# Kernel optimization log

Measured on AMD Instinct MI355X. Metric: run time of the kernel, lower is better.

Reference implementation:

```python
import jax, jax.numpy as jnp
import numpy as np

B, U, CV, IN, H = 256, 64, 61, 3, 1024
NG, NAG = 20, 10
G = 4 * H  # LSTM gate width (i,f,g,o)


def _lstm_cell(x, h, c, Wih, Whh, bih, bhh):
    # PyTorch LSTM gate order: i, f, g, o
    g = x @ Wih.T + h @ Whh.T + bih + bhh
    i, f, gg, o = jnp.split(g, 4, axis=-1)
    c2 = jax.nn.sigmoid(f) * c + jax.nn.sigmoid(i) * jnp.tanh(gg)
    h2 = jax.nn.sigmoid(o) * jnp.tanh(c2)
    return h2, c2


def _bilstm(x, h, c, pf, pb):
    # Bidirectional LSTM over a length-1 sequence: one cell step per direction.
    hf, cf = _lstm_cell(x, h[0], c[0], *pf)
    hb, cb = _lstm_cell(x, h[1], c[1], *pb)
    return jnp.concatenate([hf, hb], axis=-1), jnp.stack([hf, hb]), jnp.stack([cf, cb])


def _forward(inp, char_vec, old_k, old_w, h1, c1, h2, c2, params, text_len):
    (Wih1f, Whh1f, bih1f, bhh1f, Wih1b, Whh1b, bih1b, bhh1b,
     Wih2f, Whh2f, bih2f, bhh2f, Wih2b, Whh2b, bih2b, bhh2b,
     W_win, b_win, W_mdn, b_mdn) = params
    # embed = cat([inp, old_w]) over the feature dim; seq len is 1 so squeeze it.
    x1 = jnp.concatenate([inp[:, 0], old_w[:, 0]], axis=-1)          # [B, IN+CV]
    out1, h1n, c1n = _bilstm(x1, h1, c1,
                             (Wih1f, Whh1f, bih1f, bhh1f),
                             (Wih1b, Whh1b, bih1b, bhh1b))           # [B, 2H]
    # Gaussian-mixture attention window (Graves 2013)
    abk = jnp.exp(out1 @ W_win.T + b_win)                            # [B, 3*NAG]
    a_t, b_t, k_t = jnp.split(abk, 3, axis=1)
    k_t = old_k + k_t
    u = jnp.arange(1, U + 1, dtype=jnp.float32)                      # [U]
    phi_bku = jnp.exp(-b_t[:, :, None] * (k_t[:, :, None] - u) ** 2) # [B,NAG,U]
    phi = jnp.einsum('bk,bku->bu', a_t, phi_bku) * (float(U) / text_len)
    win = jnp.einsum('bu,buc->bc', phi, char_vec)                    # [B, CV]
    # Second LSTM with skip connections
    x2 = jnp.concatenate([out1, inp[:, 0], win], axis=-1)            # [B, 2H+IN+CV]
    out2, h2n, c2n = _bilstm(x2, h2, c2,
                             (Wih2f, Whh2f, bih2f, bhh2f),
                             (Wih2b, Whh2b, bih2b, bhh2b))           # [B, 2H]
    # Mixture-density output head
    y = jnp.concatenate([out1, out2], axis=-1) @ W_mdn.T + b_mdn     # [B, 6*NG+1]
    e = jax.nn.sigmoid(y[:, :1])
    pi, mu1, mu2, s1, s2, rho = jnp.split(y[:, 1:], 6, axis=1)
    pi = jax.nn.softmax(pi, axis=1)  # bias = 0 default
    return (e, pi, mu1, mu2, jnp.exp(s1), jnp.exp(s2), jnp.tanh(rho),
            phi, win, k_t, h1n, c1n, h2n, c2n)


def setup_inputs() -> dict:
    key = jax.random.key(0)
    ks = jax.random.split(key, 32)
    def w(k, shape):
        return jax.random.normal(k, shape, dtype=jnp.float32) * 0.02
    d = {
        'inp': jax.random.normal(ks[0], (B, 1, IN), dtype=jnp.float32),
        'char_vec': jax.random.uniform(ks[1], (B, U, CV), dtype=jnp.float32),
        'old_k': jax.random.uniform(ks[2], (B, NAG), dtype=jnp.float32),
        'old_w': jax.random.uniform(ks[3], (B, 1, CV), dtype=jnp.float32),
        'h1': jnp.zeros((2, B, H), jnp.float32),
        'c1': jnp.zeros((2, B, H), jnp.float32),
        'h2': jnp.zeros((2, B, H), jnp.float32),
        'c2': jnp.zeros((2, B, H), jnp.float32),
        'text_len': 64,
    }
    in1 = IN + CV          # rnn1 input width = 64
    in2 = 2 * H + IN + CV  # rnn2 input width = 2112
    i = 4
    for pre, ind in [('1f', in1), ('1b', in1), ('2f', in2), ('2b', in2)]:
        d['Wih' + pre] = w(ks[i], (G, ind)); i += 1
        d['Whh' + pre] = w(ks[i], (G, H)); i += 1
        d['bih' + pre] = w(ks[i], (G,)); i += 1
        d['bhh' + pre] = w(ks[i], (G,)); i += 1
    d['W_win'] = w(ks[i], (3 * NAG, 2 * H)); i += 1
    d['b_win'] = w(ks[i], (3 * NAG,)) - 2.0; i += 1  # keep exp(abk) moderate
    d['W_mdn'] = w(ks[i], (6 * NG + 1, 4 * H)); i += 1
    d['b_mdn'] = w(ks[i], (6 * NG + 1,))
    return d


def reference(inp, char_vec, old_k, old_w, h1, c1, h2, c2, text_len,
              Wih1f, Whh1f, bih1f, bhh1f, Wih1b, Whh1b, bih1b, bhh1b,
              Wih2f, Whh2f, bih2f, bhh2f, Wih2b, Whh2b, bih2b, bhh2b,
              W_win, b_win, W_mdn, b_mdn):
    params = (Wih1f, Whh1f, bih1f, bhh1f, Wih1b, Whh1b, bih1b, bhh1b,
              Wih2f, Whh2f, bih2f, bhh2f, Wih2b, Whh2b, bih2b, bhh2b,
              W_win, b_win, W_mdn, b_mdn)
    return _forward(inp, char_vec, old_k, old_w, h1, c1, h2, c2, params, text_len)
```

## Files before the change

### kernel.cpp

```cpp
#include <hip/hip_runtime.h>

#define Bsz 256
#define Usz 64
#define CVsz 61
#define INsz 3
#define Hsz 1024
#define Gsz 4096
#define NGsz 20
#define NAGsz 10
#define IN2sz 2112

typedef __attribute__((ext_vector_type(8))) short bf16x8;
typedef __attribute__((ext_vector_type(4))) float f32x4;
typedef __attribute__((ext_vector_type(4))) unsigned int u32x4;

__device__ __forceinline__ unsigned int pk2(float x, float y) {
  unsigned int a = __float_as_uint(x), b = __float_as_uint(y);
  return ((a + 0x8000u) >> 16) | ((b + 0x8000u) & 0xffff0000u);
}

__device__ __forceinline__ float sigf(float x) { return 1.f / (1.f + __expf(-x)); }

struct GemmP {
  const float* X1; int ldx1; int nc1; int ldw1;
  const float* Wf1; const float* Wb1;
  const float* Hst; const float* Wf2; const float* Wb2;
  const float* bihf; const float* bhhf; const float* bihb; const float* bhhb;
  float* gout;
  int ksplit; int totc; int ndir; int nW; int ldo;
};

__global__ __launch_bounds__(256) void gemm_k(GemmP p) {
  __shared__ __align__(16) unsigned short As[128 * 32];
  __shared__ __align__(16) unsigned short Bs[128 * 32];
  int t = threadIdx.x;
  int n0 = blockIdx.x * 128, m0 = blockIdx.y * 128;
  int z = blockIdx.z;
  int d = (p.ndir == 2) ? (z & 1) : 0;
  int s = (p.ndir == 2) ? (z >> 1) : z;
  const float* Wih = d ? p.Wb1 : p.Wf1;
  const float* Whh = d ? p.Wb2 : p.Wf2;
  const float* Hx = p.Hst + (size_t)d * Bsz * Hsz;
  int c0 = (p.totc * s) / p.ksplit, c1 = (p.totc * (s + 1)) / p.ksplit;
  int wv = t >> 6, ln = t & 63;
  int wr = wv >> 1, wc = wv & 1;
  int fr = ln & 15, kg = ln >> 4;
  int sr = t >> 1, skp = (t & 1) * 16;

  f32x4 acc[4][4];
#pragma unroll
  for (int i = 0; i < 4; i++)
#pragma unroll
    for (int j = 0; j < 4; j++) acc[i][j] = (f32x4){0.f, 0.f, 0.f, 0.f};

  for (int c = c0; c < c1; ++c) {
    const float* Xp; int ldx, kx; const float* Wp; int ldw;
    if (c < p.nc1) { Xp = p.X1; ldx = p.ldx1; kx = c * 32; Wp = Wih; ldw = p.ldw1; }
    else           { Xp = Hx;   ldx = Hsz;    kx = (c - p.nc1) * 32; Wp = Whh; ldw = Hsz; }

    const float* ax = Xp + (size_t)(m0 + sr) * ldx + kx + skp;
    float4 a0 = *(const float4*)(ax);
    float4 a1 = *(const float4*)(ax + 4);
    float4 a2 = *(const float4*)(ax + 8);
    float4 a3 = *(const float4*)(ax + 12);
    int rw = n0 + sr; if (rw >= p.nW) rw = p.nW - 1;
    const float* bx = Wp + (size_t)rw * ldw + kx + skp;
    float4 b0 = *(const float4*)(bx);
    float4 b1 = *(const float4*)(bx + 4);
    float4 b2 = *(const float4*)(bx + 8);
    float4 b3 = *(const float4*)(bx + 12);

    __syncthreads();
    *(u32x4*)(&As[sr * 32 + skp])     = (u32x4){pk2(a0.x, a0.y), pk2(a0.z, a0.w), pk2(a1.x, a1.y), pk2(a1.z, a1.w)};
    *(u32x4*)(&As[sr * 32 + skp + 8]) = (u32x4){pk2(a2.x, a2.y), pk2(a2.z, a2.w), pk2(a3.x, a3.y), pk2(a3.z, a3.w)};
    *(u32x4*)(&Bs[sr * 32 + skp])     = (u32x4){pk2(b0.x, b0.y), pk2(b0.z, b0.w), pk2(b1.x, b1.y), pk2(b1.z, b1.w)};
    *(u32x4*)(&Bs[sr * 32 + skp + 8]) = (u32x4){pk2(b2.x, b2.y), pk2(b2.z, b2.w), pk2(b3.x, b3.y), pk2(b3.z, b3.w)};
    __syncthreads();

    const unsigned short* Ab = &As[(wr * 64 + fr) * 32 + kg * 8];
    const unsigned short* Bb = &Bs[(wc * 64 + fr) * 32 + kg * 8];
    bf16x8 av[4], bv[4];
#pragma unroll
    for (int i = 0; i < 4; i++) av[i] = *(const bf16x8*)(Ab + i * 16 * 32);
#pragma unroll
    for (int j = 0; j < 4; j++) bv[j] = *(const bf16x8*)(Bb + j * 16 * 32);
#pragma unroll
    for (int i = 0; i < 4; i++)
#pragma unroll
      for (int j = 0; j < 4; j++)
        acc[i][j] = __builtin_amdgcn_mfma_f32_16x16x32_bf16(av[i], bv[j], acc[i][j], 0, 0, 0);
  }

  const float* bi = d ? p.bihb : p.bihf;
  const float* bh = d ? p.bhhb : p.bhhf;
  float* outp = p.gout + (size_t)(s * p.ndir + d) * Bsz * p.ldo;
#pragma unroll
  for (int i = 0; i < 4; i++) {
#pragma unroll
    for (int j = 0; j < 4; j++) {
      int col = n0 + wc * 64 + j * 16 + fr;
      float bias = 0.f;
      if (p.bihf && s == 0) bias = bi[col] + bh[col];
#pragma unroll
      for (int r = 0; r < 4; r++) {
        int row = m0 + wr * 64 + i * 16 + kg * 4 + r;
        outp[(size_t)row * p.ldo + col] = acc[i][j][r] + bias;
      }
    }
  }
}

__global__ __launch_bounds__(256) void prep_x1(const float* inp, const float* oldw, float* x1) {
  int idx = blockIdx.x * 256 + threadIdx.x;
  int m = idx >> 6, k = idx & 63;
  x1[idx] = (k < INsz) ? inp[m * INsz + k] : oldw[m * CVsz + (k - INsz)];
}

__global__ __launch_bounds__(256) void cell_k(const float* gates, int ksplit,
    const float* cin, float* hout, float* cout,
    float* dst1, int ld1, int off1, float* dst2, int ld2, int off2) {
  int idx = blockIdx.x * 256 + threadIdx.x;
  int j = idx & (Hsz - 1);
  int m = (idx >> 10) & 255;
  int d = idx >> 18;
  size_t base = ((size_t)d * Bsz + m) * Gsz + j;
  float gi = 0.f, gf = 0.f, gg = 0.f, go = 0.f;
  for (int s = 0; s < ksplit; ++s) {
    const float* gp = gates + (size_t)s * 2 * Bsz * Gsz + base;
    gi += gp[0]; gf += gp[1024]; gg += gp[2048]; go += gp[3072];
  }
  float c = cin[((size_t)d * Bsz + m) * Hsz + j];
  float cn = sigf(gf) * c + sigf(gi) * tanhf(gg);
  float hn = sigf(go) * tanhf(cn);
  hout[((size_t)d * Bsz + m) * Hsz + j] = hn;
  cout[((size_t)d * Bsz + m) * Hsz + j] = cn;
  dst1[(size_t)m * ld1 + off1 + d * Hsz + j] = hn;
  if (dst2) dst2[(size_t)m * ld2 + off2 + d * Hsz + j] = hn;
}

__global__ __launch_bounds__(128) void win_fin(const float* winp, int ks,
    const float* bwin, const float* oldk, const float* inp, const float* cvec,
    const int* tl, float* x2w, float* ophi, float* owin, float* okt) {
  int m = blockIdx.x, t = threadIdx.x, wv = t >> 6, ln = t & 63;
  __shared__ float abk[30];
  __shared__ float phis[Usz];
  __shared__ float wpart[2][CVsz];
  if (t < 30) {
    float s = bwin[t];
    for (int q = 0; q < ks; ++q) s += winp[((size_t)q * Bsz + m) * 128 + t];
    abk[t] = __expf(s);
  }
  __syncthreads();
  if (t < NAGsz) {
    float kt = oldk[m * NAGsz + t] + abk[20 + t];
    abk[20 + t] = kt;
    okt[m * NAGsz + t] = kt;
  }
  __syncthreads();
  if (t < Usz) {
    float scale = 64.f / (float)tl[0];
    float ph = 0.f;
#pragma unroll
    for (int q = 0; q < NAGsz; ++q) {
      float dk = abk[20 + q] - (float)(t + 1);
      ph += abk[q] * __expf(-abk[10 + q] * dk * dk);
    }
    ph *= scale;
    phis[t] = ph;
    ophi[m * Usz + t] = ph;
  }
  __syncthreads();
  if (ln < CVsz) {
    float w = 0.f;
    const float* cv = cvec + (size_t)m * Usz * CVsz + (size_t)wv * 32 * CVsz + ln;
#pragma unroll
    for (int u = 0; u < 32; ++u) w += phis[wv * 32 + u] * cv[u * CVsz];
    wpart[wv][ln] = w;
  }
  __syncthreads();
  if (t < CVsz) {
    float w = wpart[0][t] + wpart[1][t];
    owin[m * CVsz + t] = w;
    x2w[(size_t)m * IN2sz + 2048 + INsz + t] = w;
  }
  if (t < INsz) x2w[(size_t)m * IN2sz + 2048 + t] = inp[m * INsz + t];
}

__global__ __launch_bounds__(128) void mdn_fin(const float* part, int ks, const float* bm, float* out) {
  int m = blockIdx.x, t = threadIdx.x;
  __shared__ float y[121];
  if (t < 121) {
    float s = bm[t];
    for (int q = 0; q < ks; ++q) s += part[((size_t)q * Bsz + m) * 128 + t];
    y[t] = s;
  }
  __syncthreads();
  if (t == 0) out[m] = sigf(y[0]);
  if (t < NGsz) {
    float mx = -1e30f;
    for (int q = 0; q < NGsz; q++) mx = fmaxf(mx, y[1 + q]);
    float se = 0.f;
    for (int q = 0; q < NGsz; q++) se += __expf(y[1 + q] - mx);
    out[256   + m * NGsz + t] = __expf(y[1 + t] - mx) / se;
    out[5376  + m * NGsz + t] = y[21 + t];
    out[10496 + m * NGsz + t] = y[41 + t];
    out[15616 + m * NGsz + t] = __expf(y[61 + t]);
    out[20736 + m * NGsz + t] = __expf(y[81 + t]);
    out[25856 + m * NGsz + t] = tanhf(y[101 + t]);
  }
}

extern "C" void kernel_launch(void* const* d_in, const int* in_sizes, int n_in,
                              void* d_out, int out_size, void* d_ws, size_t ws_size,
                              hipStream_t stream) {
  (void)in_sizes; (void)n_in; (void)out_size;
  const float* inp  = (const float*)d_in[0];
  const float* cvec = (const float*)d_in[1];
  const float* oldk = (const float*)d_in[2];
  const float* oldw = (const float*)d_in[3];
  const float* h1   = (const float*)d_in[4];
  const float* c1   = (const float*)d_in[5];
  const float* h2   = (const float*)d_in[6];
  const float* c2   = (const float*)d_in[7];
  const int*   tl   = (const int*)d_in[8];
  float* out = (float*)d_out;
  float* ws  = (float*)d_ws;

  float* ws_x1   = ws;
  float* ws_x2   = ws + 16384;
  float* ws_cat  = ws_x2 + 540672;
  float* ws_mdn  = ws_cat + 1048576;
  float* ws_winp = ws_mdn + 262144;
  float* ws_g    = ws_winp + 262144;

  size_t fixed = (size_t)16384 + 540672 + 1048576 + 262144 + 262144;
  int ksplit = 4;
  while (ksplit > 1 && (fixed + (size_t)ksplit * 2 * 1048576) * 4 > ws_size) ksplit >>= 1;

  prep_x1<<<64, 256, 0, stream>>>(inp, oldw, ws_x1);

  GemmP g1{};
  g1.X1 = ws_x1; g1.ldx1 = 64; g1.nc1 = 2; g1.ldw1 = 64;
  g1.Wf1 = (const float*)d_in[9];  g1.Wb1 = (const float*)d_in[13];
  g1.Hst = h1; g1.Wf2 = (const float*)d_in[10]; g1.Wb2 = (const float*)d_in[14];
  g1.bihf = (const float*)d_in[11]; g1.bhhf = (const float*)d_in[12];
  g1.bihb = (const float*)d_in[15]; g1.bhhb = (const float*)d_in[16];
  g1.gout = ws_g; g1.ksplit = ksplit; g1.totc = 34; g1.ndir = 2; g1.nW = 4096; g1.ldo = 4096;
  gemm_k<<<dim3(32, 2, 2 * ksplit), 256, 0, stream>>>(g1);

  cell_k<<<2048, 256, 0, stream>>>(ws_g, ksplit, c1, out + 65536, out + 589824,
                                   ws_x2, IN2sz, 0, ws_cat, 4096, 0);

  GemmP gw{};
  gw.X1 = ws_x2; gw.ldx1 = IN2sz; gw.nc1 = 64; gw.ldw1 = 2048;
  gw.Wf1 = (const float*)d_in[25]; gw.Wb1 = (const float*)d_in[25];
  gw.Hst = ws_x2; gw.Wf2 = (const float*)d_in[25]; gw.Wb2 = (const float*)d_in[25];
  gw.bihf = nullptr; gw.bhhf = nullptr; gw.bihb = nullptr; gw.bhhb = nullptr;
  gw.gout = ws_winp; gw.ksplit = 8; gw.totc = 64; gw.ndir = 1; gw.nW = 30; gw.ldo = 128;
  gemm_k<<<dim3(1, 2, 8), 256, 0, stream>>>(gw);

  win_fin<<<256, 128, 0, stream>>>(ws_winp, 8, (const float*)d_in[26],
                                   oldk, inp, cvec, tl, ws_x2,
                                   out + 30976, out + 47360, out + 62976);

  GemmP g2{};
  g2.X1 = ws_x2; g2.ldx1 = IN2sz; g2.nc1 = 66; g2.ldw1 = IN2sz;
  g2.Wf1 = (const float*)d_in[17]; g2.Wb1 = (const float*)d_in[21];
  g2.Hst = h2; g2.Wf2 = (const float*)d_in[18]; g2.Wb2 = (const float*)d_in[22];
  g2.bihf = (const float*)d_in[19]; g2.bhhf = (const float*)d_in[20];
  g2.bihb = (const float*)d_in[23]; g2.bhhb = (const float*)d_in[24];
  g2.gout = ws_g; g2.ksplit = ksplit; g2.totc = 98; g2.ndir = 2; g2.nW = 4096; g2.ldo = 4096;
  gemm_k<<<dim3(32, 2, 2 * ksplit), 256, 0, stream>>>(g2);

  cell_k<<<2048, 256, 0, stream>>>(ws_g, ksplit, c2, out + 1114112, out + 1638400,
                                   ws_cat, 4096, 2048, nullptr, 0, 0);

  GemmP gm{};
  gm.X1 = ws_cat; gm.ldx1 = 4096; gm.nc1 = 128; gm.ldw1 = 4096;
  gm.Wf1 = (const float*)d_in[27]; gm.Wb1 = (const float*)d_in[27];
  gm.Hst = ws_cat; gm.Wf2 = ws_cat; gm.Wb2 = ws_cat;
  gm.bihf = nullptr; gm.bhhf = nullptr; gm.bihb = nullptr; gm.bhhb = nullptr;
  gm.gout = ws_mdn; gm.ksplit = 8; gm.totc = 128; gm.ndir = 1; gm.nW = 121; gm.ldo = 128;
  gemm_k<<<dim3(1, 2, 8), 256, 0, stream>>>(gm);

  mdn_fin<<<256, 128, 0, stream>>>(ws_mdn, 8, (const float*)d_in[28], out);
}
```

Baseline: 314.6 us.

## Double-buffer GEMM shared tiles with padding and raise split-K factors

The GEMM main loop now uses two padded LDS buffers. The global loads for the next K chunk are issued before the MFMA work on the current chunk, and only one barrier is needed per iteration. Row padding to 40 elements is meant to cut LDS bank conflicts on the fragment reads. Split-K doubles for the LSTM gate GEMMs and the small window and MDN GEMMs to put more blocks in flight. This costs larger workspace partials and more reduction traffic in the cell and finalize kernels.

```diff
diff --git a/kernel.cpp b/kernel.cpp
--- a/kernel.cpp
+++ b/kernel.cpp
@@ -9,6 +9,7 @@
 #define NGsz 20
 #define NAGsz 10
 #define IN2sz 2112
+#define LDP 40
 
 typedef __attribute__((ext_vector_type(8))) short bf16x8;
 typedef __attribute__((ext_vector_type(4))) float f32x4;
@@ -30,9 +31,9 @@
   int ksplit; int totc; int ndir; int nW; int ldo;
 };
 
-__global__ __launch_bounds__(256) void gemm_k(GemmP p) {
-  __shared__ __align__(16) unsigned short As[128 * 32];
-  __shared__ __align__(16) unsigned short Bs[128 * 32];
+__global__ __launch_bounds__(256, 4) void gemm_k(GemmP p) {
+  __shared__ __align__(16) unsigned short As[2][128 * LDP];
+  __shared__ __align__(16) unsigned short Bs[2][128 * LDP];
   int t = threadIdx.x;
   int n0 = blockIdx.x * 128, m0 = blockIdx.y * 128;
   int z = blockIdx.z;
@@ -53,43 +54,57 @@
 #pragma unroll
     for (int j = 0; j < 4; j++) acc[i][j] = (f32x4){0.f, 0.f, 0.f, 0.f};
 
-  for (int c = c0; c < c1; ++c) {
+  float4 a0, a1, a2, a3, b0, b1, b2, b3;
+
+  auto LOAD = [&](int c) {
     const float* Xp; int ldx, kx; const float* Wp; int ldw;
     if (c < p.nc1) { Xp = p.X1; ldx = p.ldx1; kx = c * 32; Wp = Wih; ldw = p.ldw1; }
     else           { Xp = Hx;   ldx = Hsz;    kx = (c - p.nc1) * 32; Wp = Whh; ldw = Hsz; }
-
     const float* ax = Xp + (size_t)(m0 + sr) * ldx + kx + skp;
-    float4 a0 = *(const float4*)(ax);
-    float4 a1 = *(const float4*)(ax + 4);
-    float4 a2 = *(const float4*)(ax + 8);
-    float4 a3 = *(const float4*)(ax + 12);
+    a0 = *(const float4*)(ax);
+    a1 = *(const float4*)(ax + 4);
+    a2 = *(const float4*)(ax + 8);
+    a3 = *(const float4*)(ax + 12);
     int rw = n0 + sr; if (rw >= p.nW) rw = p.nW - 1;
     const float* bx = Wp + (size_t)rw * ldw + kx + skp;
-    float4 b0 = *(const float4*)(bx);
-    float4 b1 = *(const float4*)(bx + 4);
-    float4 b2 = *(const float4*)(bx + 8);
-    float4 b3 = *(const float4*)(bx + 12);
-
-    __syncthreads();
-    *(u32x4*)(&As[sr * 32 + skp])     = (u32x4){pk2(a0.x, a0.y), pk2(a0.z, a0.w), pk2(a1.x, a1.y), pk2(a1.z, a1.w)};
-    *(u32x4*)(&As[sr * 32 + skp + 8]) = (u32x4){pk2(a2.x, a2.y), pk2(a2.z, a2.w), pk2(a3.x, a3.y), pk2(a3.z, a3.w)};
-    *(u32x4*)(&Bs[sr * 32 + skp])     = (u32x4){pk2(b0.x, b0.y), pk2(b0.z, b0.w), pk2(b1.x, b1.y), pk2(b1.z, b1.w)};
-    *(u32x4*)(&Bs[sr * 32 + skp + 8]) = (u32x4){pk2(b2.x, b2.y), pk2(b2.z, b2.w), pk2(b3.x, b3.y), pk2(b3.z, b3.w)};
-    __syncthreads();
-
-    const unsigned short* Ab = &As[(wr * 64 + fr) * 32 + kg * 8];
-    const unsigned short* Bb = &Bs[(wc * 64 + fr) * 32 + kg * 8];
+    b0 = *(const float4*)(bx);
+    b1 = *(const float4*)(bx + 4);
+    b2 = *(const float4*)(bx + 8);
+    b3 = *(const float4*)(bx + 12);
+  };
+  auto STORE = [&](int buf) {
+    *(u32x4*)(&As[buf][sr * LDP + skp])     = (u32x4){pk2(a0.x, a0.y), pk2(a0.z, a0.w), pk2(a1.x, a1.y), pk2(a1.z, a1.w)};
+    *(u32x4*)(&As[buf][sr * LDP + skp + 8]) = (u32x4){pk2(a2.x, a2.y), pk2(a2.z, a2.w), pk2(a3.x, a3.y), pk2(a3.z, a3.w)};
+    *(u32x4*)(&Bs[buf][sr * LDP + skp])     = (u32x4){pk2(b0.x, b0.y), pk2(b0.z, b0.w), pk2(b1.x, b1.y), pk2(b1.z, b1.w)};
+    *(u32x4*)(&Bs[buf][sr * LDP + skp + 8]) = (u32x4){pk2(b2.x, b2.y), pk2(b2.z, b2.w), pk2(b3.x, b3.y), pk2(b3.z, b3.w)};
+  };
+  auto MFMA = [&](int buf) {
+    const unsigned short* Ab = &As[buf][(wr * 64 + fr) * LDP + kg * 8];
+    const unsigned short* Bb = &Bs[buf][(wc * 64 + fr) * LDP + kg * 8];
     bf16x8 av[4], bv[4];
 #pragma unroll
-    for (int i = 0; i < 4; i++) av[i] = *(const bf16x8*)(Ab + i * 16 * 32);
-#pragma unroll
-    for (int j = 0; j < 4; j++) bv[j] = *(const bf16x8*)(Bb + j * 16 * 32);
+    for (int i = 0; i < 4; i++) av[i] = *(const bf16x8*)(Ab + i * 16 * LDP);
+#pragma unroll
+    for (int j = 0; j < 4; j++) bv[j] = *(const bf16x8*)(Bb + j * 16 * LDP);
 #pragma unroll
     for (int i = 0; i < 4; i++)
 #pragma unroll
       for (int j = 0; j < 4; j++)
         acc[i][j] = __builtin_amdgcn_mfma_f32_16x16x32_bf16(av[i], bv[j], acc[i][j], 0, 0, 0);
-  }
+  };
+
+  LOAD(c0);
+  STORE(0);
+  __syncthreads();
+  int cur = 0;
+  for (int c = c0 + 1; c < c1; ++c) {
+    LOAD(c);
+    MFMA(cur);
+    STORE(cur ^ 1);
+    __syncthreads();
+    cur ^= 1;
+  }
+  MFMA(cur);
 
   const float* bi = d ? p.bihb : p.bihf;
   const float* bh = d ? p.bhhb : p.bhhf;
@@ -230,11 +245,11 @@
   float* ws_x2   = ws + 16384;
   float* ws_cat  = ws_x2 + 540672;
   float* ws_mdn  = ws_cat + 1048576;
-  float* ws_winp = ws_mdn + 262144;
-  float* ws_g    = ws_winp + 262144;
-
-  size_t fixed = (size_t)16384 + 540672 + 1048576 + 262144 + 262144;
-  int ksplit = 4;
+  float* ws_winp = ws_mdn + 524288;
+  float* ws_g    = ws_winp + 524288;
+
+  size_t fixed = (size_t)16384 + 540672 + 1048576 + 524288 + 524288;
+  int ksplit = 8;
   while (ksplit > 1 && (fixed + (size_t)ksplit * 2 * 1048576) * 4 > ws_size) ksplit >>= 1;
 
   prep_x1<<<64, 256, 0, stream>>>(inp, oldw, ws_x1);
@@ -256,10 +271,10 @@
   gw.Wf1 = (const float*)d_in[25]; gw.Wb1 = (const float*)d_in[25];
   gw.Hst = ws_x2; gw.Wf2 = (const float*)d_in[25]; gw.Wb2 = (const float*)d_in[25];
   gw.bihf = nullptr; gw.bhhf = nullptr; gw.bihb = nullptr; gw.bhhb = nullptr;
-  gw.gout = ws_winp; gw.ksplit = 8; gw.totc = 64; gw.ndir = 1; gw.nW = 30; gw.ldo = 128;
-  gemm_k<<<dim3(1, 2, 8), 256, 0, stream>>>(gw);
-
-  win_fin<<<256, 128, 0, stream>>>(ws_winp, 8, (const float*)d_in[26],
+  gw.gout = ws_winp; gw.ksplit = 16; gw.totc = 64; gw.ndir = 1; gw.nW = 30; gw.ldo = 128;
+  gemm_k<<<dim3(1, 2, 16), 256, 0, stream>>>(gw);
+
+  win_fin<<<256, 128, 0, stream>>>(ws_winp, 16, (const float*)d_in[26],
                                    oldk, inp, cvec, tl, ws_x2,
                                    out + 30976, out + 47360, out + 62976);
 
@@ -280,8 +295,8 @@
   gm.Wf1 = (const float*)d_in[27]; gm.Wb1 = (const float*)d_in[27];
   gm.Hst = ws_cat; gm.Wf2 = ws_cat; gm.Wb2 = ws_cat;
   gm.bihf = nullptr; gm.bhhf = nullptr; gm.bihb = nullptr; gm.bhhb = nullptr;
-  gm.gout = ws_mdn; gm.ksplit = 8; gm.totc = 128; gm.ndir = 1; gm.nW = 121; gm.ldo = 128;
-  gemm_k<<<dim3(1, 2, 8), 256, 0, stream>>>(gm);
-
-  mdn_fin<<<256, 128, 0, stream>>>(ws_mdn, 8, (const float*)d_in[28], out);
-}
+  gm.gout = ws_mdn; gm.ksplit = 16; gm.totc = 128; gm.ndir = 1; gm.nW = 121; gm.ldo = 128;
+  gemm_k<<<dim3(1, 2, 16), 256, 0, stream>>>(gm);
+
+  mdn_fin<<<256, 128, 0, stream>>>(ws_mdn, 16, (const float*)d_in[28], out);
+}
```

Measured after the change: 336.9 us. 1.07x slower.

## Double-buffer GEMM LDS tiles with K=64 chunks, padding and register prefetch

Applied to the files above, without the earlier changes.

The GEMM kernel now processes 64-wide K chunks instead of 32, uses double-buffered padded LDS tiles (stride 72 to reduce bank conflicts), and prefetches the next chunk's global loads into registers while MFMAs run on the current buffer, leaving one barrier per iteration. Chunk counts in the host launches are halved to match, and the first LSTM GEMM uses a smaller k-split. The aim is to hide global-load latency and cut synchronisation overhead. In exchange it needs more registers (16 float4 staging) and more LDS, which may limit occupancy despite the launch bound hint.

```diff
diff --git a/kernel.cpp b/kernel.cpp
--- a/kernel.cpp
+++ b/kernel.cpp
@@ -9,6 +9,7 @@
 #define NGsz 20
 #define NAGsz 10
 #define IN2sz 2112
+#define LDP 72
 
 typedef __attribute__((ext_vector_type(8))) short bf16x8;
 typedef __attribute__((ext_vector_type(4))) float f32x4;
@@ -30,9 +31,9 @@
   int ksplit; int totc; int ndir; int nW; int ldo;
 };
 
-__global__ __launch_bounds__(256) void gemm_k(GemmP p) {
-  __shared__ __align__(16) unsigned short As[128 * 32];
-  __shared__ __align__(16) unsigned short Bs[128 * 32];
+__global__ __launch_bounds__(256, 2) void gemm_k(GemmP p) {
+  __shared__ __align__(16) unsigned short As[2][128 * LDP];
+  __shared__ __align__(16) unsigned short Bs[2][128 * LDP];
   int t = threadIdx.x;
   int n0 = blockIdx.x * 128, m0 = blockIdx.y * 128;
   int z = blockIdx.z;
@@ -45,7 +46,7 @@
   int wv = t >> 6, ln = t & 63;
   int wr = wv >> 1, wc = wv & 1;
   int fr = ln & 15, kg = ln >> 4;
-  int sr = t >> 1, skp = (t & 1) * 16;
+  int srow = t >> 1, shalf = t & 1;
 
   f32x4 acc[4][4];
 #pragma unroll
@@ -53,43 +54,67 @@
 #pragma unroll
     for (int j = 0; j < 4; j++) acc[i][j] = (f32x4){0.f, 0.f, 0.f, 0.f};
 
-  for (int c = c0; c < c1; ++c) {
+  float4 ar[8], br[8];
+
+  auto LOADR = [&](int c) {
     const float* Xp; int ldx, kx; const float* Wp; int ldw;
-    if (c < p.nc1) { Xp = p.X1; ldx = p.ldx1; kx = c * 32; Wp = Wih; ldw = p.ldw1; }
-    else           { Xp = Hx;   ldx = Hsz;    kx = (c - p.nc1) * 32; Wp = Whh; ldw = Hsz; }
-
-    const float* ax = Xp + (size_t)(m0 + sr) * ldx + kx + skp;
-    float4 a0 = *(const float4*)(ax);
-    float4 a1 = *(const float4*)(ax + 4);
-    float4 a2 = *(const float4*)(ax + 8);
-    float4 a3 = *(const float4*)(ax + 12);
-    int rw = n0 + sr; if (rw >= p.nW) rw = p.nW - 1;
-    const float* bx = Wp + (size_t)rw * ldw + kx + skp;
-    float4 b0 = *(const float4*)(bx);
-    float4 b1 = *(const float4*)(bx + 4);
-    float4 b2 = *(const float4*)(bx + 8);
-    float4 b3 = *(const float4*)(bx + 12);
-
+    if (c < p.nc1) { Xp = p.X1; ldx = p.ldx1; kx = c * 64; Wp = Wih; ldw = p.ldw1; }
+    else           { Xp = Hx;   ldx = Hsz;    kx = (c - p.nc1) * 64; Wp = Whh; ldw = Hsz; }
+    const float* ax = Xp + (size_t)(m0 + srow) * ldx + kx + shalf * 32;
+#pragma unroll
+    for (int q = 0; q < 8; q++) ar[q] = *(const float4*)(ax + 4 * q);
+    int rw = n0 + srow; if (rw >= p.nW) rw = p.nW - 1;
+    const float* bx = Wp + (size_t)rw * ldw + kx + shalf * 32;
+#pragma unroll
+    for (int q = 0; q < 8; q++) br[q] = *(const float4*)(bx + 4 * q);
+  };
+  auto DSW = [&](int buf) {
+    unsigned short* pa = &As[buf][srow * LDP + shalf * 32];
+    unsigned short* pb = &Bs[buf][srow * LDP + shalf * 32];
+#pragma unroll
+    for (int q = 0; q < 4; q++) {
+      *(u32x4*)(pa + q * 8) = (u32x4){pk2(ar[2*q].x, ar[2*q].y), pk2(ar[2*q].z, ar[2*q].w),
+                                      pk2(ar[2*q+1].x, ar[2*q+1].y), pk2(ar[2*q+1].z, ar[2*q+1].w)};
+    }
+#pragma unroll
+    for (int q = 0; q < 4; q++) {
+      *(u32x4*)(pb + q * 8) = (u32x4){pk2(br[2*q].x, br[2*q].y), pk2(br[2*q].z, br[2*q].w),
+                                      pk2(br[2*q+1].x, br[2*q+1].y), pk2(br[2*q+1].z, br[2*q+1].w)};
+    }
+  };
+  auto MFMA = [&](int buf) {
+    const unsigned short* Ab = &As[buf][(wr * 64 + fr) * LDP + kg * 8];
+    const unsigned short* Bb = &Bs[buf][(wc * 64 + fr) * LDP + kg * 8];
+    bf16x8 av[2][4], bv[2][4];
+#pragma unroll
+    for (int kk = 0; kk < 2; kk++) {
+#pragma unroll
+      for (int i = 0; i < 4; i++) av[kk][i] = *(const bf16x8*)(Ab + i * 16 * LDP + kk * 32);
+#pragma unroll
+      for (int j = 0; j < 4; j++) bv[kk][j] = *(const bf16x8*)(Bb + j * 16 * LDP + kk * 32);
+    }
+#pragma unroll
+    for (int kk = 0; kk < 2; kk++)
+#pragma unroll
+      for (int i = 0; i < 4; i++)
+#pragma unroll
+        for (int j = 0; j < 4; j++)
+          acc[i][j] = __builtin_amdgcn_mfma_f32_16x16x32_bf16(av[kk][i], bv[kk][j], acc[i][j], 0, 0, 0);
+  };
+
+  LOADR(c0);
+  DSW(0);
+  __syncthreads();
+  int cur = 0;
+  for (int c = c0 + 1; c < c1; ++c) {
+    LOADR(c);
+    __builtin_amdgcn_sched_barrier(0);
+    MFMA(cur);
+    DSW(cur ^ 1);
     __syncthreads();
-    *(u32x4*)(&As[sr * 32 + skp])     = (u32x4){pk2(a0.x, a0.y), pk2(a0.z, a0.w), pk2(a1.x, a1.y), pk2(a1.z, a1.w)};
-    *(u32x4*)(&As[sr * 32 + skp + 8]) = (u32x4){pk2(a2.x, a2.y), pk2(a2.z, a2.w), pk2(a3.x, a3.y), pk2(a3.z, a3.w)};
-    *(u32x4*)(&Bs[sr * 32 + skp])     = (u32x4){pk2(b0.x, b0.y), pk2(b0.z, b0.w), pk2(b1.x, b1.y), pk2(b1.z, b1.w)};
-    *(u32x4*)(&Bs[sr * 32 + skp + 8]) = (u32x4){pk2(b2.x, b2.y), pk2(b2.z, b2.w), pk2(b3.x, b3.y), pk2(b3.z, b3.w)};
-    __syncthreads();
-
-    const unsigned short* Ab = &As[(wr * 64 + fr) * 32 + kg * 8];
-    const unsigned short* Bb = &Bs[(wc * 64 + fr) * 32 + kg * 8];
-    bf16x8 av[4], bv[4];
-#pragma unroll
-    for (int i = 0; i < 4; i++) av[i] = *(const bf16x8*)(Ab + i * 16 * 32);
-#pragma unroll
-    for (int j = 0; j < 4; j++) bv[j] = *(const bf16x8*)(Bb + j * 16 * 32);
-#pragma unroll
-    for (int i = 0; i < 4; i++)
-#pragma unroll
-      for (int j = 0; j < 4; j++)
-        acc[i][j] = __builtin_amdgcn_mfma_f32_16x16x32_bf16(av[i], bv[j], acc[i][j], 0, 0, 0);
-  }
+    cur ^= 1;
+  }
+  MFMA(cur);
 
   const float* bi = d ? p.bihb : p.bihf;
   const float* bh = d ? p.bhhb : p.bhhf;
@@ -234,29 +259,30 @@
   float* ws_g    = ws_winp + 262144;
 
   size_t fixed = (size_t)16384 + 540672 + 1048576 + 262144 + 262144;
-  int ksplit = 4;
-  while (ksplit > 1 && (fixed + (size_t)ksplit * 2 * 1048576) * 4 > ws_size) ksplit >>= 1;
+  int ks2 = 4;
+  while (ks2 > 1 && (fixed + (size_t)ks2 * 2 * 1048576) * 4 > ws_size) ks2 >>= 1;
+  int ks1 = ks2 < 2 ? 1 : 2;
 
   prep_x1<<<64, 256, 0, stream>>>(inp, oldw, ws_x1);
 
   GemmP g1{};
-  g1.X1 = ws_x1; g1.ldx1 = 64; g1.nc1 = 2; g1.ldw1 = 64;
+  g1.X1 = ws_x1; g1.ldx1 = 64; g1.nc1 = 1; g1.ldw1 = 64;
   g1.Wf1 = (const float*)d_in[9];  g1.Wb1 = (const float*)d_in[13];
   g1.Hst = h1; g1.Wf2 = (const float*)d_in[10]; g1.Wb2 = (const float*)d_in[14];
   g1.bihf = (const float*)d_in[11]; g1.bhhf = (const float*)d_in[12];
   g1.bihb = (const float*)d_in[15]; g1.bhhb = (const float*)d_in[16];
-  g1.gout = ws_g; g1.ksplit = ksplit; g1.totc = 34; g1.ndir = 2; g1.nW = 4096; g1.ldo = 4096;
-  gemm_k<<<dim3(32, 2, 2 * ksplit), 256, 0, stream>>>(g1);
-
-  cell_k<<<2048, 256, 0, stream>>>(ws_g, ksplit, c1, out + 65536, out + 589824,
+  g1.gout = ws_g; g1.ksplit = ks1; g1.totc = 17; g1.ndir = 2; g1.nW = 4096; g1.ldo = 4096;
+  gemm_k<<<dim3(32, 2, 2 * ks1), 256, 0, stream>>>(g1);
+
+  cell_k<<<2048, 256, 0, stream>>>(ws_g, ks1, c1, out + 65536, out + 589824,
                                    ws_x2, IN2sz, 0, ws_cat, 4096, 0);
 
   GemmP gw{};
-  gw.X1 = ws_x2; gw.ldx1 = IN2sz; gw.nc1 = 64; gw.ldw1 = 2048;
+  gw.X1 = ws_x2; gw.ldx1 = IN2sz; gw.nc1 = 32; gw.ldw1 = 2048;
   gw.Wf1 = (const float*)d_in[25]; gw.Wb1 = (const float*)d_in[25];
   gw.Hst = ws_x2; gw.Wf2 = (const float*)d_in[25]; gw.Wb2 = (const float*)d_in[25];
   gw.bihf = nullptr; gw.bhhf = nullptr; gw.bihb = nullptr; gw.bhhb = nullptr;
-  gw.gout = ws_winp; gw.ksplit = 8; gw.totc = 64; gw.ndir = 1; gw.nW = 30; gw.ldo = 128;
+  gw.gout = ws_winp; gw.ksplit = 8; gw.totc = 32; gw.ndir = 1; gw.nW = 30; gw.ldo = 128;
   gemm_k<<<dim3(1, 2, 8), 256, 0, stream>>>(gw);
 
   win_fin<<<256, 128, 0, stream>>>(ws_winp, 8, (const float*)d_in[26],
@@ -264,23 +290,23 @@
                                    out + 30976, out + 47360, out + 62976);
 
   GemmP g2{};
-  g2.X1 = ws_x2; g2.ldx1 = IN2sz; g2.nc1 = 66; g2.ldw1 = IN2sz;
+  g2.X1 = ws_x2; g2.ldx1 = IN2sz; g2.nc1 = 33; g2.ldw1 = IN2sz;
   g2.Wf1 = (const float*)d_in[17]; g2.Wb1 = (const float*)d_in[21];
   g2.Hst = h2; g2.Wf2 = (const float*)d_in[18]; g2.Wb2 = (const float*)d_in[22];
   g2.bihf = (const float*)d_in[19]; g2.bhhf = (const float*)d_in[20];
   g2.bihb = (const float*)d_in[23]; g2.bhhb = (const float*)d_in[24];
-  g2.gout = ws_g; g2.ksplit = ksplit; g2.totc = 98; g2.ndir = 2; g2.nW = 4096; g2.ldo = 4096;
-  gemm_k<<<dim3(32, 2, 2 * ksplit), 256, 0, stream>>>(g2);
-
-  cell_k<<<2048, 256, 0, stream>>>(ws_g, ksplit, c2, out + 1114112, out + 1638400,
+  g2.gout = ws_g; g2.ksplit = ks2; g2.totc = 49; g2.ndir = 2; g2.nW = 4096; g2.ldo = 4096;
+  gemm_k<<<dim3(32, 2, 2 * ks2), 256, 0, stream>>>(g2);
+
+  cell_k<<<2048, 256, 0, stream>>>(ws_g, ks2, c2, out + 1114112, out + 1638400,
                                    ws_cat, 4096, 2048, nullptr, 0, 0);
 
   GemmP gm{};
-  gm.X1 = ws_cat; gm.ldx1 = 4096; gm.nc1 = 128; gm.ldw1 = 4096;
+  gm.X1 = ws_cat; gm.ldx1 = 4096; gm.nc1 = 64; gm.ldw1 = 4096;
   gm.Wf1 = (const float*)d_in[27]; gm.Wb1 = (const float*)d_in[27];
   gm.Hst = ws_cat; gm.Wf2 = ws_cat; gm.Wb2 = ws_cat;
   gm.bihf = nullptr; gm.bhhf = nullptr; gm.bihb = nullptr; gm.bhhb = nullptr;
-  gm.gout = ws_mdn; gm.ksplit = 8; gm.totc = 128; gm.ndir = 1; gm.nW = 121; gm.ldo = 128;
+  gm.gout = ws_mdn; gm.ksplit = 8; gm.totc = 64; gm.ndir = 1; gm.nW = 121; gm.ldo = 128;
   gemm_k<<<dim3(1, 2, 8), 256, 0, stream>>>(gm);
 
   mdn_fin<<<256, 128, 0, stream>>>(ws_mdn, 8, (const float*)d_in[28], out);
```

Result: slower. 342.1 us (+8.8%).

## Drop LDS staging in GEMM; load bf16 activations and packed weights directly into MFMA fragments

Applied to the files above, without the earlier changes.

The GEMM kernel no longer stages A/B tiles through shared memory with two barriers per k-step. Each lane now loads its MFMA fragment straight from global memory: activations come from buffers pre-converted to bf16 by new conversion kernels and by cell_k/win_fin, and weights are read as fp32 and packed to bf16 in registers. The goal is to remove LDS traffic and synchronisation and to halve the activation read volume. In exchange each weight row is now fetched redundantly by several waves, three extra conversion launches are added, and the split-K factor for the small window and MDN GEMMs goes from 8 to 16.

```diff
diff --git a/kernel.cpp b/kernel.cpp
--- a/kernel.cpp
+++ b/kernel.cpp
@@ -18,21 +18,27 @@
   unsigned int a = __float_as_uint(x), b = __float_as_uint(y);
   return ((a + 0x8000u) >> 16) | ((b + 0x8000u) & 0xffff0000u);
 }
-
+__device__ __forceinline__ unsigned short bf1(float x) {
+  return (unsigned short)((__float_as_uint(x) + 0x8000u) >> 16);
+}
+__device__ __forceinline__ bf16x8 pkb(float4 lo, float4 hi) {
+  union { u32x4 u; bf16x8 b; } cv;
+  cv.u = (u32x4){pk2(lo.x, lo.y), pk2(lo.z, lo.w), pk2(hi.x, hi.y), pk2(hi.z, hi.w)};
+  return cv.b;
+}
 __device__ __forceinline__ float sigf(float x) { return 1.f / (1.f + __expf(-x)); }
 
 struct GemmP {
-  const float* X1; int ldx1; int nc1; int ldw1;
-  const float* Wf1; const float* Wb1;
-  const float* Hst; const float* Wf2; const float* Wb2;
+  const unsigned short* X1; int ldx1; int nc1;
+  const unsigned short* Hst;
+  const float* Wf1; const float* Wb1; int ldw1;
+  const float* Wf2; const float* Wb2;
   const float* bihf; const float* bhhf; const float* bihb; const float* bhhb;
   float* gout;
   int ksplit; int totc; int ndir; int nW; int ldo;
 };
 
 __global__ __launch_bounds__(256) void gemm_k(GemmP p) {
-  __shared__ __align__(16) unsigned short As[128 * 32];
-  __shared__ __align__(16) unsigned short Bs[128 * 32];
   int t = threadIdx.x;
   int n0 = blockIdx.x * 128, m0 = blockIdx.y * 128;
   int z = blockIdx.z;
@@ -40,12 +46,20 @@
   int s = (p.ndir == 2) ? (z >> 1) : z;
   const float* Wih = d ? p.Wb1 : p.Wf1;
   const float* Whh = d ? p.Wb2 : p.Wf2;
-  const float* Hx = p.Hst + (size_t)d * Bsz * Hsz;
+  const unsigned short* Hx = p.Hst + (size_t)d * Bsz * Hsz;
   int c0 = (p.totc * s) / p.ksplit, c1 = (p.totc * (s + 1)) / p.ksplit;
   int wv = t >> 6, ln = t & 63;
   int wr = wv >> 1, wc = wv & 1;
   int fr = ln & 15, kg = ln >> 4;
-  int sr = t >> 1, skp = (t & 1) * 16;
+
+  int rA[4], rB[4];
+#pragma unroll
+  for (int i = 0; i < 4; i++) rA[i] = m0 + wr * 64 + i * 16 + fr;
+#pragma unroll
+  for (int j = 0; j < 4; j++) {
+    int r = n0 + wc * 64 + j * 16 + fr;
+    rB[j] = (r < p.nW) ? r : (p.nW - 1);
+  }
 
   f32x4 acc[4][4];
 #pragma unroll
@@ -53,37 +67,39 @@
 #pragma unroll
     for (int j = 0; j < 4; j++) acc[i][j] = (f32x4){0.f, 0.f, 0.f, 0.f};
 
-  for (int c = c0; c < c1; ++c) {
-    const float* Xp; int ldx, kx; const float* Wp; int ldw;
-    if (c < p.nc1) { Xp = p.X1; ldx = p.ldx1; kx = c * 32; Wp = Wih; ldw = p.ldw1; }
-    else           { Xp = Hx;   ldx = Hsz;    kx = (c - p.nc1) * 32; Wp = Whh; ldw = Hsz; }
-
-    const float* ax = Xp + (size_t)(m0 + sr) * ldx + kx + skp;
-    float4 a0 = *(const float4*)(ax);
-    float4 a1 = *(const float4*)(ax + 4);
-    float4 a2 = *(const float4*)(ax + 8);
-    float4 a3 = *(const float4*)(ax + 12);
-    int rw = n0 + sr; if (rw >= p.nW) rw = p.nW - 1;
-    const float* bx = Wp + (size_t)rw * ldw + kx + skp;
-    float4 b0 = *(const float4*)(bx);
-    float4 b1 = *(const float4*)(bx + 4);
-    float4 b2 = *(const float4*)(bx + 8);
-    float4 b3 = *(const float4*)(bx + 12);
-
-    __syncthreads();
-    *(u32x4*)(&As[sr * 32 + skp])     = (u32x4){pk2(a0.x, a0.y), pk2(a0.z, a0.w), pk2(a1.x, a1.y), pk2(a1.z, a1.w)};
-    *(u32x4*)(&As[sr * 32 + skp + 8]) = (u32x4){pk2(a2.x, a2.y), pk2(a2.z, a2.w), pk2(a3.x, a3.y), pk2(a3.z, a3.w)};
-    *(u32x4*)(&Bs[sr * 32 + skp])     = (u32x4){pk2(b0.x, b0.y), pk2(b0.z, b0.w), pk2(b1.x, b1.y), pk2(b1.z, b1.w)};
-    *(u32x4*)(&Bs[sr * 32 + skp + 8]) = (u32x4){pk2(b2.x, b2.y), pk2(b2.z, b2.w), pk2(b3.x, b3.y), pk2(b3.z, b3.w)};
-    __syncthreads();
-
-    const unsigned short* Ab = &As[(wr * 64 + fr) * 32 + kg * 8];
-    const unsigned short* Bb = &Bs[(wc * 64 + fr) * 32 + kg * 8];
+  int e1 = (c1 < p.nc1) ? c1 : p.nc1;
+#pragma unroll 2
+  for (int c = c0; c < e1; ++c) {
+    int kx = c * 32 + kg * 8;
     bf16x8 av[4], bv[4];
 #pragma unroll
-    for (int i = 0; i < 4; i++) av[i] = *(const bf16x8*)(Ab + i * 16 * 32);
-#pragma unroll
-    for (int j = 0; j < 4; j++) bv[j] = *(const bf16x8*)(Bb + j * 16 * 32);
+    for (int i = 0; i < 4; i++)
+      av[i] = *(const bf16x8*)(p.X1 + (size_t)rA[i] * p.ldx1 + kx);
+#pragma unroll
+    for (int j = 0; j < 4; j++) {
+      const float* wp = Wih + (size_t)rB[j] * p.ldw1 + kx;
+      bv[j] = pkb(*(const float4*)wp, *(const float4*)(wp + 4));
+    }
+#pragma unroll
+    for (int i = 0; i < 4; i++)
+#pragma unroll
+      for (int j = 0; j < 4; j++)
+        acc[i][j] = __builtin_amdgcn_mfma_f32_16x16x32_bf16(av[i], bv[j], acc[i][j], 0, 0, 0);
+  }
+
+  int s2 = (c0 > p.nc1) ? c0 : p.nc1;
+#pragma unroll 2
+  for (int c = s2; c < c1; ++c) {
+    int kx = (c - p.nc1) * 32 + kg * 8;
+    bf16x8 av[4], bv[4];
+#pragma unroll
+    for (int i = 0; i < 4; i++)
+      av[i] = *(const bf16x8*)(Hx + (size_t)rA[i] * Hsz + kx);
+#pragma unroll
+    for (int j = 0; j < 4; j++) {
+      const float* wp = Whh + (size_t)rB[j] * Hsz + kx;
+      bv[j] = pkb(*(const float4*)wp, *(const float4*)(wp + 4));
+    }
 #pragma unroll
     for (int i = 0; i < 4; i++)
 #pragma unroll
@@ -110,15 +126,21 @@
   }
 }
 
-__global__ __launch_bounds__(256) void prep_x1(const float* inp, const float* oldw, float* x1) {
+__global__ __launch_bounds__(256) void prep_x1b(const float* inp, const float* oldw, unsigned short* x1b) {
   int idx = blockIdx.x * 256 + threadIdx.x;
   int m = idx >> 6, k = idx & 63;
-  x1[idx] = (k < INsz) ? inp[m * INsz + k] : oldw[m * CVsz + (k - INsz)];
+  float v = (k < INsz) ? inp[m * INsz + k] : oldw[m * CVsz + (k - INsz)];
+  x1b[idx] = bf1(v);
+}
+
+__global__ __launch_bounds__(256) void cvt_h(const float* h, unsigned short* hb, int n) {
+  int idx = blockIdx.x * 256 + threadIdx.x;
+  if (idx < n) hb[idx] = bf1(h[idx]);
 }
 
 __global__ __launch_bounds__(256) void cell_k(const float* gates, int ksplit,
     const float* cin, float* hout, float* cout,
-    float* dst1, int ld1, int off1, float* dst2, int ld2, int off2) {
+    unsigned short* db1, int ld1, int off1, unsigned short* db2, int ld2, int off2) {
   int idx = blockIdx.x * 256 + threadIdx.x;
   int j = idx & (Hsz - 1);
   int m = (idx >> 10) & 255;
@@ -134,13 +156,14 @@
   float hn = sigf(go) * tanhf(cn);
   hout[((size_t)d * Bsz + m) * Hsz + j] = hn;
   cout[((size_t)d * Bsz + m) * Hsz + j] = cn;
-  dst1[(size_t)m * ld1 + off1 + d * Hsz + j] = hn;
-  if (dst2) dst2[(size_t)m * ld2 + off2 + d * Hsz + j] = hn;
+  unsigned short hb = bf1(hn);
+  db1[(size_t)m * ld1 + off1 + d * Hsz + j] = hb;
+  if (db2) db2[(size_t)m * ld2 + off2 + d * Hsz + j] = hb;
 }
 
 __global__ __launch_bounds__(128) void win_fin(const float* winp, int ks,
     const float* bwin, const float* oldk, const float* inp, const float* cvec,
-    const int* tl, float* x2w, float* ophi, float* owin, float* okt) {
+    const int* tl, unsigned short* x2b, float* ophi, float* owin, float* okt) {
   int m = blockIdx.x, t = threadIdx.x, wv = t >> 6, ln = t & 63;
   __shared__ float abk[30];
   __shared__ float phis[Usz];
@@ -181,9 +204,9 @@
   if (t < CVsz) {
     float w = wpart[0][t] + wpart[1][t];
     owin[m * CVsz + t] = w;
-    x2w[(size_t)m * IN2sz + 2048 + INsz + t] = w;
-  }
-  if (t < INsz) x2w[(size_t)m * IN2sz + 2048 + t] = inp[m * INsz + t];
+    x2b[(size_t)m * IN2sz + 2048 + INsz + t] = bf1(w);
+  }
+  if (t < INsz) x2b[(size_t)m * IN2sz + 2048 + t] = bf1(inp[m * INsz + t]);
 }
 
 __global__ __launch_bounds__(128) void mdn_fin(const float* part, int ks, const float* bm, float* out) {
@@ -226,62 +249,72 @@
   float* out = (float*)d_out;
   float* ws  = (float*)d_ws;
 
-  float* ws_x1   = ws;
-  float* ws_x2   = ws + 16384;
-  float* ws_cat  = ws_x2 + 540672;
-  float* ws_mdn  = ws_cat + 1048576;
-  float* ws_winp = ws_mdn + 262144;
-  float* ws_g    = ws_winp + 262144;
-
-  size_t fixed = (size_t)16384 + 540672 + 1048576 + 262144 + 262144;
-  int ksplit = 4;
-  while (ksplit > 1 && (fixed + (size_t)ksplit * 2 * 1048576) * 4 > ws_size) ksplit >>= 1;
-
-  prep_x1<<<64, 256, 0, stream>>>(inp, oldw, ws_x1);
+  size_t fixed_f = (size_t)524288 + 524288 + 8192 + 262144 + 262144 + 270336 + 524288;
+  int ks2 = 4;
+  while (ks2 > 1 && (fixed_f + (size_t)ks2 * 2 * 1048576) * 4 > ws_size) ks2 >>= 1;
+  int ks1 = 4;
+
+  float* ws_g    = ws;
+  float* ws_mdn  = ws_g + (size_t)ks2 * 2 * 1048576;
+  float* ws_winp = ws_mdn + 524288;
+  float* bstart  = ws_winp + 524288;
+  unsigned short* x1b  = (unsigned short*)bstart;
+  unsigned short* h1b  = x1b + 16384;
+  unsigned short* h2b  = h1b + 524288;
+  unsigned short* x2b  = h2b + 524288;
+  unsigned short* catb = x2b + 540672;
+
+  prep_x1b<<<64, 256, 0, stream>>>(inp, oldw, x1b);
+  cvt_h<<<2048, 256, 0, stream>>>(h1, h1b, 524288);
+  cvt_h<<<2048, 256, 0, stream>>>(h2, h2b, 524288);
 
   GemmP g1{};
-  g1.X1 = ws_x1; g1.ldx1 = 64; g1.nc1 = 2; g1.ldw1 = 64;
-  g1.Wf1 = (const float*)d_in[9];  g1.Wb1 = (const float*)d_in[13];
-  g1.Hst = h1; g1.Wf2 = (const float*)d_in[10]; g1.Wb2 = (const float*)d_in[14];
+  g1.X1 = x1b; g1.ldx1 = 64; g1.nc1 = 2;
+  g1.Hst = h1b;
+  g1.Wf1 = (const float*)d_in[9];  g1.Wb1 = (const float*)d_in[13]; g1.ldw1 = 64;
+  g1.Wf2 = (const float*)d_in[10]; g1.Wb2 = (const float*)d_in[14];
   g1.bihf = (const float*)d_in[11]; g1.bhhf = (const float*)d_in[12];
   g1.bihb = (const float*)d_in[15]; g1.bhhb = (const float*)d_in[16];
-  g1.gout = ws_g; g1.ksplit = ksplit; g1.totc = 34; g1.ndir = 2; g1.nW = 4096; g1.ldo = 4096;
-  gemm_k<<<dim3(32, 2, 2 * ksplit), 256, 0, stream>>>(g1);
-
-  cell_k<<<2048, 256, 0, stream>>>(ws_g, ksplit, c1, out + 65536, out + 589824,
-                                   ws_x2, IN2sz, 0, ws_cat, 4096, 0);
+  g1.gout = ws_g; g1.ksplit = ks1; g1.totc = 34; g1.ndir = 2; g1.nW = 4096; g1.ldo = 4096;
+  gemm_k<<<dim3(32, 2, 2 * ks1), 256, 0, stream>>>(g1);
+
+  cell_k<<<2048, 256, 0, stream>>>(ws_g, ks1, c1, out + 65536, out + 589824,
+                                   x2b, IN2sz, 0, catb, 4096, 0);
 
   GemmP gw{};
-  gw.X1 = ws_x2; gw.ldx1 = IN2sz; gw.nc1 = 64; gw.ldw1 = 2048;
-  gw.Wf1 = (const float*)d_in[25]; gw.Wb1 = (const float*)d_in[25];
-  gw.Hst = ws_x2; gw.Wf2 = (const float*)d_in[25]; gw.Wb2 = (const float*)d_in[25];
+  gw.X1 = x2b; gw.ldx1 = IN2sz; gw.nc1 = 64;
+  gw.Hst = x2b;
+  gw.Wf1 = (const float*)d_in[25]; gw.Wb1 = (const float*)d_in[25]; gw.ldw1 = 2048;
+  gw.Wf2 = (const float*)d_in[25]; gw.Wb2 = (const float*)d_in[25];
   gw.bihf = nullptr; gw.bhhf = nullptr; gw.bihb = nullptr; gw.bhhb = nullptr;
-  gw.gout = ws_winp; gw.ksplit = 8; gw.totc = 64; gw.ndir = 1; gw.nW = 30; gw.ldo = 128;
-  gemm_k<<<dim3(1, 2, 8), 256, 0, stream>>>(gw);
-
-  win_fin<<<256, 128, 0, stream>>>(ws_winp, 8, (const float*)d_in[26],
-                                   oldk, inp, cvec, tl, ws_x2,
+  gw.gout = ws_winp; gw.ksplit = 16; gw.totc = 64; gw.ndir = 1; gw.nW = 30; gw.ldo = 128;
+  gemm_k<<<dim3(1, 2, 16), 256, 0, stream>>>(gw);
+
+  win_fin<<<256, 128, 0, stream>>>(ws_winp, 16, (const float*)d_in[26],
+                                   oldk, inp, cvec, tl, x2b,
                                    out + 30976, out + 47360, out + 62976);
 
   GemmP g2{};
-  g2.X1 = ws_x2; g2.ldx1 = IN2sz; g2.nc1 = 66; g2.ldw1 = IN2sz;
-  g2.Wf1 = (const float*)d_in[17]; g2.Wb1 = (const float*)d_in[21];
-  g2.Hst = h2; g2.Wf2 = (const float*)d_in[18]; g2.Wb2 = (const float*)d_in[22];
+  g2.X1 = x2b; g2.ldx1 = IN2sz; g2.nc1 = 66;
+  g2.Hst = h2b;
+  g2.Wf1 = (const float*)d_in[17]; g2.Wb1 = (const float*)d_in[21]; g2.ldw1 = IN2sz;
+  g2.Wf2 = (const float*)d_in[18]; g2.Wb2 = (const float*)d_in[22];
   g2.bihf = (const float*)d_in[19]; g2.bhhf = (const float*)d_in[20];
   g2.bihb = (const float*)d_in[23]; g2.bhhb = (const float*)d_in[24];
-  g2.gout = ws_g; g2.ksplit = ksplit; g2.totc = 98; g2.ndir = 2; g2.nW = 4096; g2.ldo = 4096;
-  gemm_k<<<dim3(32, 2, 2 * ksplit), 256, 0, stream>>>(g2);
-
-  cell_k<<<2048, 256, 0, stream>>>(ws_g, ksplit, c2, out + 1114112, out + 1638400,
-                                   ws_cat, 4096, 2048, nullptr, 0, 0);
+  g2.gout = ws_g; g2.ksplit = ks2; g2.totc = 98; g2.ndir = 2; g2.nW = 4096; g2.ldo = 4096;
+  gemm_k<<<dim3(32, 2, 2 * ks2), 256, 0, stream>>>(g2);
+
+  cell_k<<<2048, 256, 0, stream>>>(ws_g, ks2, c2, out + 1114112, out + 1638400,
+                                   catb, 4096, 2048, nullptr, 0, 0);
 
   GemmP gm{};
-  gm.X1 = ws_cat; gm.ldx1 = 4096; gm.nc1 = 128; gm.ldw1 = 4096;
-  gm.Wf1 = (const float*)d_in[27]; gm.Wb1 = (const float*)d_in[27];
-  gm.Hst = ws_cat; gm.Wf2 = ws_cat; gm.Wb2 = ws_cat;
+  gm.X1 = catb; gm.ldx1 = 4096; gm.nc1 = 128;
+  gm.Hst = catb;
+  gm.Wf1 = (const float*)d_in[27]; gm.Wb1 = (const float*)d_in[27]; gm.ldw1 = 4096;
+  gm.Wf2 = (const float*)d_in[27]; gm.Wb2 = (const float*)d_in[27];
   gm.bihf = nullptr; gm.bhhf = nullptr; gm.bihb = nullptr; gm.bhhb = nullptr;
-  gm.gout = ws_mdn; gm.ksplit = 8; gm.totc = 128; gm.ndir = 1; gm.nW = 121; gm.ldo = 128;
-  gemm_k<<<dim3(1, 2, 8), 256, 0, stream>>>(gm);
-
-  mdn_fin<<<256, 128, 0, stream>>>(ws_mdn, 8, (const float*)d_in[28], out);
-}
+  gm.gout = ws_mdn; gm.ksplit = 16; gm.totc = 128; gm.ndir = 1; gm.nW = 121; gm.ldo = 128;
+  gemm_k<<<dim3(1, 2, 16), 256, 0, stream>>>(gm);
+
+  mdn_fin<<<256, 128, 0, stream>>>(ws_mdn, 16, (const float*)d_in[28], out);
+}
```

Measured after the change: 348.7 us. 1.11x slower.
